# Kernel tuning notes

Hardware: AMD Instinct MI355X
Metric: run time of the kernel (lower is better)

The kernel has to match this reference:

```python
import jax, jax.numpy as jnp
import numpy as np


def _lstm_layer(x_seq, h0, c0, Wih, Whh, bih, bhh):
    """Standard (PyTorch-gate-order: i, f, g, o) LSTM over a [T, B, C] sequence."""
    b = bih + bhh  # [4H]
    # Precompute input projections for all timesteps at once: [T, B, 4H]
    x_proj = jnp.einsum('tbc,gc->tbg', x_seq, Wih) + b

    def step(carry, xp_t):
        h, c = carry
        gates = xp_t + h @ Whh.T  # [B, 4H]
        i, f, g, o = jnp.split(gates, 4, axis=-1)
        i = jax.nn.sigmoid(i)
        f = jax.nn.sigmoid(f)
        g = jnp.tanh(g)
        o = jax.nn.sigmoid(o)
        c_new = f * c + i * g
        h_new = o * jnp.tanh(c_new)
        return (h_new, c_new), h_new

    (hT, cT), ys = jax.lax.scan(step, (h0, c0), x_proj)
    return ys, hT, cT


def setup_inputs() -> dict:
    key = jax.random.key(0)
    ks = jax.random.split(key, 16)
    T, B, C, H = 1024, 64, 256, 512
    s_in = 1.0 / np.sqrt(H)
    inp = {
        'x': jax.random.normal(ks[0], (T, B, C), jnp.float32),
        'h0_0': jax.random.normal(ks[1], (B, H), jnp.float32) * 0.1,
        'c0_0': jax.random.normal(ks[2], (B, H), jnp.float32) * 0.1,
        'h0_1': jax.random.normal(ks[3], (B, H), jnp.float32) * 0.1,
        'c0_1': jax.random.normal(ks[4], (B, H), jnp.float32) * 0.1,
        'Wih0': jax.random.normal(ks[5], (4 * H, C), jnp.float32) * s_in,
        'Whh0': jax.random.normal(ks[6], (4 * H, H), jnp.float32) * s_in,
        'bih0': jax.random.normal(ks[7], (4 * H,), jnp.float32) * s_in,
        'bhh0': jax.random.normal(ks[8], (4 * H,), jnp.float32) * s_in,
        'Wih1': jax.random.normal(ks[9], (4 * H, H), jnp.float32) * s_in,
        'Whh1': jax.random.normal(ks[10], (4 * H, H), jnp.float32) * s_in,
        'bih1': jax.random.normal(ks[11], (4 * H,), jnp.float32) * s_in,
        'bhh1': jax.random.normal(ks[12], (4 * H,), jnp.float32) * s_in,
    }
    return inp


def reference(x, h0_0, c0_0, h0_1, c0_1, Wih0, Whh0, bih0, bhh0, Wih1, Whh1, bih1, bhh1):
    # Layer 0 over the full sequence, then layer 1 consumes its outputs.
    # Mathematically identical to the original timestep-major Python loop.
    y0, h1f, c1f = _lstm_layer(x, h0_0, c0_0, Wih0, Whh0, bih0, bhh0)
    y1, h2f, c2f = _lstm_layer(y0, h0_1, c0_1, Wih1, Whh1, bih1, bhh1)
    return (y1, h1f, c1f, h2f, c2f)
```

## Files before the change

kernel.cpp:

```cpp
#include <hip/hip_runtime.h>


#define TT 1024
#define BB 64
#define CC 256
#define HH 512
#define Y_ELEMS (TT * BB * HH)
#define S_ELEMS (BB * HH)

typedef __attribute__((ext_vector_type(8))) short bf16x8;
typedef __attribute__((ext_vector_type(4))) float f32x4;
typedef unsigned int u32;
typedef unsigned short u16;
typedef unsigned long long u64;

#define WS_BAR 0
#define WS_CNT 32768
#define WS_BSUM0 36864
#define WS_BSUM1 45056
#define WS_H0 53248
#define WS_H1 184320
#define WS_WPK0 315392
#define WS_WPK1 3461120

__device__ __forceinline__ u16 f2b_rne(float f) {
    u32 u = __float_as_uint(f);
    return (u16)((u + 0x7FFFu + ((u >> 16) & 1u)) >> 16);
}
__device__ __forceinline__ u16 f2b_fast(float f) {
    return (u16)((__float_as_uint(f) + 0x8000u) >> 16);
}
__device__ __forceinline__ float sigf(float z) { return 1.0f / (1.0f + __expf(-z)); }
__device__ __forceinline__ float tanh_f(float z) { return 2.0f / (1.0f + __expf(-2.0f * z)) - 1.0f; }

__device__ __forceinline__ bf16x8 pack8(float4 a, float4 b) {
    union { u16 u[8]; bf16x8 v; } r;
    r.u[0] = f2b_fast(a.x); r.u[1] = f2b_fast(a.y); r.u[2] = f2b_fast(a.z); r.u[3] = f2b_fast(a.w);
    r.u[4] = f2b_fast(b.x); r.u[5] = f2b_fast(b.y); r.u[6] = f2b_fast(b.z); r.u[7] = f2b_fast(b.w);
    return r.v;
}

__device__ __forceinline__ u32 ld_u32_sc(const u32* p) {
    return __hip_atomic_load(p, __ATOMIC_RELAXED, __HIP_MEMORY_SCOPE_AGENT);
}
__device__ __forceinline__ void add_u32_sc(u32* p, u32 v) {
    (void)__hip_atomic_fetch_add(p, v, __ATOMIC_RELAXED, __HIP_MEMORY_SCOPE_AGENT);
}

__global__ void k_init(const float* __restrict__ bih0, const float* __restrict__ bhh0,
                       const float* __restrict__ bih1, const float* __restrict__ bhh1,
                       const float* __restrict__ h00, const float* __restrict__ h01,
                       unsigned char* __restrict__ ws) {
    u32* bar = (u32*)(ws + WS_BAR);
    float* bs0 = (float*)(ws + WS_BSUM0);
    float* bs1 = (float*)(ws + WS_BSUM1);
    u16* h0 = (u16*)(ws + WS_H0);
    u16* h1 = (u16*)(ws + WS_H1);
    int t = blockIdx.x * 256 + threadIdx.x;
    if (t < 8704) bar[t] = 0u;
    if (t < 2048) { bs0[t] = bih0[t] + bhh0[t]; bs1[t] = bih1[t] + bhh1[t]; }
    if (t < S_ELEMS) {
        int b = t >> 9, col = t & 511;
        int no = ((col >> 4) << 10) + (b << 4) + (col & 15);
        h0[no] = f2b_rne(h00[t]);
        h1[no] = f2b_rne(h01[t]);
    }
}

__global__ void k_wprep(const float* __restrict__ Wih0, const float* __restrict__ Whh0,
                        const float* __restrict__ Wih1, const float* __restrict__ Whh1,
                        unsigned char* __restrict__ ws) {
    u16* wpk0 = (u16*)(ws + WS_WPK0);
    u16* wpk1 = (u16*)(ws + WS_WPK1);
    int u = blockIdx.x * 256 + threadIdx.x;
    const float* s;
    u16* d;
    if (u < 128 * 24 * 64) {
        int bidL = u / (24 * 64);
        int kt = (u >> 6) % 24;
        int lane = u & 63;
        int n = lane & 15, quad = lane >> 4;
        int row = (n >> 2) * 512 + bidL * 4 + (n & 3);
        int k = kt * 32 + quad * 8;
        s = (k < 256) ? (Wih0 + (size_t)row * 256 + k) : (Whh0 + (size_t)row * 512 + (k - 256));
        d = wpk0 + (size_t)((bidL * 24 + kt) * 64 + lane) * 8;
    } else {
        int v = u - 128 * 24 * 64;
        int bidL = v / (32 * 64);
        int kt = (v >> 6) % 32;
        int lane = v & 63;
        int n = lane & 15, quad = lane >> 4;
        int row = (n >> 2) * 512 + bidL * 4 + (n & 3);
        int k = kt * 32 + quad * 8;
        s = (k < 512) ? (Wih1 + (size_t)row * 512 + k) : (Whh1 + (size_t)row * 512 + (k - 512));
        d = wpk1 + (size_t)((bidL * 32 + kt) * 64 + lane) * 8;
    }
    #pragma unroll
    for (int i = 0; i < 8; ++i) d[i] = f2b_rne(s[i]);
}

template <int LAYER>
__device__ void run_ticks(const float* __restrict__ x, const float* __restrict__ c0,
                          float* __restrict__ out, unsigned char* __restrict__ ws,
                          int bidL, unsigned char* lds) {
    constexpr int NKT = (LAYER == 0) ? 24 : 32;
    constexpr int NL = (LAYER == 0) ? 4 : 8;
    u32* cnt = (u32*)(ws + WS_CNT);
    const float* bs = (const float*)(ws + (LAYER == 0 ? WS_BSUM0 : WS_BSUM1));
    u16* h0base = (u16*)(ws + WS_H0);
    u16* h1base = (u16*)(ws + WS_H1);
    const u16* wpk = (const u16*)(ws + (LAYER == 0 ? WS_WPK0 : WS_WPK1));

    const int bg = bidL >> 5;
    const int cg = bidL & 31;
    const int tid = threadIdx.x, lane = tid & 63, wave = tid >> 6;
    const int r16 = lane & 15, quad = lane >> 4, q8 = quad * 8;
    const int gg = r16 >> 2, jj = r16 & 3;
    const int col = cg * 16 + wave * 4 + jj;
    const int mb = quad * 4 + gg;
    const int myb = bg * 16 + mb;
    const int sl0 = (quad << 4) | (0 << 2) | jj;
    const int sl1 = (quad << 4) | (1 << 2) | jj;
    const int sl2 = (quad << 4) | (2 << 2) | jj;
    const int sl3 = (quad << 4) | (3 << 2) | jj;
    const int baseln = (quad << 4) | (gg << 2);

    u16* hstage = (u16*)(lds + 32768);
    const int sw = (r16 & 7) << 4;

    u32* gcnt = cnt + (u32)bg * 4 * 32;
    u32* mycnt = gcnt + (u32)((LAYER * 32 + cg) & 3) * 32;

    const float bi = bs[0 * HH + col], bf_ = bs[1 * HH + col];
    const float bg_ = bs[2 * HH + col], bo = bs[3 * HH + col];
    float c = c0[myb * HH + col];

    f32x4 wf[NKT];
    {
        const u16* wp = wpk + (size_t)((cg * 4 + wave) * NKT * 64 + lane) * 8;
        #pragma unroll
        for (int kt = 0; kt < NKT; ++kt) wf[kt] = *(const f32x4*)(wp + (size_t)kt * 64 * 8);
        #pragma unroll
        for (int kt = 0; kt < NKT; ++kt) asm volatile("" : "+v"(wf[kt]));
    }

    float4 xf0[8], xf1[8];
    if (LAYER == 0) {
        const float* xp = x + (size_t)(bg * 16 + r16) * CC + q8;
        #pragma unroll
        for (int kt = 0; kt < 8; ++kt) {
            xf0[kt] = *(const float4*)(xp + kt * 32);
            xf1[kt] = *(const float4*)(xp + kt * 32 + 4);
        }
    }

    for (int i = 0; i <= TT; ++i) {
        const bool active = (LAYER == 0) ? (i < TT) : (i >= 1);
        const int t = (LAYER == 0) ? i : i - 1;
        float h = 0.f;
        if (active) {
            f32x4 stg[NL];
            {
                const char* srcA = (const char*)(h0base + (size_t)((LAYER == 0 ? t : t + 1) & 1) * S_ELEMS);
                const char* srcB = (const char*)(h1base + (size_t)(t & 1) * S_ELEMS);
                #pragma unroll
                for (int k = 0; k < NL; ++k) {
                    int g = (k & 3) * 4096 + tid * 16;
                    int cgi = g >> 9;
                    int off = g & 511;
                    const char* sp = ((LAYER == 1 && k >= 4) ? srcB : srcA)
                                   + (size_t)cgi * 2048 + bg * 512 + off;
                    asm volatile("global_load_dwordx4 %0, %1, off sc0 sc1"
                                 : "=&v"(stg[k]) : "v"(sp) : "memory");
                }
            }
            f32x4 a0 = {0.f,0.f,0.f,0.f}, a1 = {0.f,0.f,0.f,0.f};
            f32x4 a2 = {0.f,0.f,0.f,0.f}, a3 = {0.f,0.f,0.f,0.f};
            if (LAYER == 0) {
                #pragma unroll
                for (int kt = 0; kt < 8; ++kt) {
                    bf16x8 a = pack8(xf0[kt], xf1[kt]);
                    bf16x8 wv = __builtin_bit_cast(bf16x8, wf[kt]);
                    f32x4& dst = (kt & 2) ? ((kt & 1) ? a3 : a2) : ((kt & 1) ? a1 : a0);
                    dst = __builtin_amdgcn_mfma_f32_16x16x32_bf16(a, wv, dst, 0, 0, 0);
                }
            }
            asm volatile("s_waitcnt vmcnt(0)" ::: "memory");
            #pragma unroll
            for (int k = 0; k < NL; ++k) {
                int g = (k & 3) * 4096 + tid * 16;
                int cgi = g >> 9;
                int off = g & 511;
                int m = off >> 5;
                int lo = (cgi * 32 + (off & 16)) ^ ((m & 7) << 4);
                int base = (LAYER == 1 && k >= 4) ? 16384 : 0;
                *(f32x4*)(lds + base + m * 1024 + lo) = stg[k];
            }
            __syncthreads();
            if (LAYER == 0) {
                #pragma unroll
                for (int kc = 0; kc < 16; kc += 8) {
                    bf16x8 av[8];
                    #pragma unroll
                    for (int j = 0; j < 8; ++j) {
                        int kt = kc + j;
                        int lo2 = (kt * 64 + quad * 16) ^ sw;
                        av[j] = *(const bf16x8*)(lds + r16 * 1024 + lo2);
                    }
                    #pragma unroll
                    for (int j = 0; j < 8; ++j) {
                        int kt = kc + j;
                        bf16x8 wv = __builtin_bit_cast(bf16x8, wf[8 + kt]);
                        f32x4& dst = (kt & 2) ? ((kt & 1) ? a3 : a2) : ((kt & 1) ? a1 : a0);
                        dst = __builtin_amdgcn_mfma_f32_16x16x32_bf16(av[j], wv, dst, 0, 0, 0);
                    }
                }
            } else {
                #pragma unroll
                for (int kc = 0; kc < 32; kc += 8) {
                    bf16x8 av[8];
                    #pragma unroll
                    for (int j = 0; j < 8; ++j) {
                        int kt = kc + j;
                        int base = (kt < 16) ? 0 : 16384;
                        int lo2 = ((kt & 15) * 64 + quad * 16) ^ sw;
                        av[j] = *(const bf16x8*)(lds + base + r16 * 1024 + lo2);
                    }
                    #pragma unroll
                    for (int j = 0; j < 8; ++j) {
                        int kt = kc + j;
                        bf16x8 wv = __builtin_bit_cast(bf16x8, wf[kt]);
                        f32x4& dst = (kt & 2) ? ((kt & 1) ? a3 : a2) : ((kt & 1) ? a1 : a0);
                        dst = __builtin_amdgcn_mfma_f32_16x16x32_bf16(av[j], wv, dst, 0, 0, 0);
                    }
                }
            }
            f32x4 acc = (a0 + a1) + (a2 + a3);

            float gi = 0.f, gf = 0.f, gc = 0.f, go = 0.f;
            #pragma unroll
            for (int r = 0; r < 4; ++r) {
                float v0 = __shfl(acc[r], sl0, 64);
                float v1 = __shfl(acc[r], sl1, 64);
                float v2 = __shfl(acc[r], sl2, 64);
                float v3 = __shfl(acc[r], sl3, 64);
                if (r == gg) { gi = v0; gf = v1; gc = v2; go = v3; }
            }
            gi = sigf(gi + bi);
            gf = sigf(gf + bf_);
            gc = tanh_f(gc + bg_);
            go = sigf(go + bo);
            c = gf * c + gi * gc;
            h = go * tanh_f(c);

            u32 w0 = f2b_rne(h);
            u32 w1 = (u32)__shfl((int)w0, baseln + 1, 64);
            u32 w2 = (u32)__shfl((int)w0, baseln + 2, 64);
            u32 w3 = (u32)__shfl((int)w0, baseln + 3, 64);
            if (jj == 0) {
                u64 pkd = (u64)(w0 | (w1 << 16)) | ((u64)(w2 | (w3 << 16)) << 32);
                *(u64*)((char*)hstage + mb * 32 + wave * 8) = pkd;
            }
        }
        if (i < TT) {
            __syncthreads();
            if (active && tid < 32) {
                u16* hw = (LAYER == 0 ? h0base : h1base) + (size_t)((t + 1) & 1) * S_ELEMS;
                f32x4 v = *(const f32x4*)((const char*)hstage + tid * 16);
                const char* dp = (const char*)hw + (size_t)cg * 2048 + bg * 512 + tid * 16;
                asm volatile("global_store_dwordx4 %0, %1, off sc0 sc1"
                             :: "v"(dp), "v"(v) : "memory");
            }
            asm volatile("s_waitcnt vmcnt(0)" ::: "memory");
            __syncthreads();
            if (tid == 0) add_u32_sc(mycnt, 1u);
        }
        if (active) {
            if (LAYER == 1) {
                float o1 = __shfl(h, baseln + 1, 64);
                float o2 = __shfl(h, baseln + 2, 64);
                float o3 = __shfl(h, baseln + 3, 64);
                if (jj == 0) {
                    float4 ov = { h, o1, o2, o3 };
                    *(float4*)(out + (size_t)t * S_ELEMS + (size_t)myb * HH
                               + cg * 16 + wave * 4) = ov;
                }
            }
            if (t == TT - 1) {
                float* fin = out + Y_ELEMS + (LAYER == 0 ? 0 : 2) * S_ELEMS;
                fin[myb * HH + col] = h;
                fin[S_ELEMS + myb * HH + col] = c;
            }
        }
        if (LAYER == 0 && i + 1 < TT) {
            const float* xp = x + ((size_t)(i + 1) * BB + bg * 16 + r16) * CC + q8;
            #pragma unroll
            for (int kt = 0; kt < 8; ++kt) {
                xf0[kt] = *(const float4*)(xp + kt * 32);
                xf1[kt] = *(const float4*)(xp + kt * 32 + 4);
            }
        }
        if (i < TT) {
            const u32 tgt = (u32)(i + 1) * 16u;
            if (tid == 0) {
                while (true) {
                    u32 v0 = ld_u32_sc(gcnt + 0 * 32);
                    u32 v1 = ld_u32_sc(gcnt + 1 * 32);
                    u32 v2 = ld_u32_sc(gcnt + 2 * 32);
                    u32 v3 = ld_u32_sc(gcnt + 3 * 32);
                    u32 m = min(min(v0, v1), min(v2, v3));
                    if (m >= tgt) break;
                }
            }
            __syncthreads();
        }
    }
}

__global__ __launch_bounds__(256) __attribute__((amdgpu_waves_per_eu(1, 1)))
void k_lstm(const float* __restrict__ x,
            const float* __restrict__ c00,
            const float* __restrict__ c01,
            float* __restrict__ out,
            unsigned char* __restrict__ ws) {
    __shared__ __align__(16) unsigned char lds[33280];
    const int bid = blockIdx.x;
    if (bid < 128) run_ticks<0>(x, c00, out, ws, bid, lds);
    else           run_ticks<1>(x, c01, out, ws, bid - 128, lds);
}

extern "C" void kernel_launch(void* const* d_in, const int* in_sizes, int n_in,
                              void* d_out, int out_size, void* d_ws, size_t ws_size,
                              hipStream_t stream) {
    const float* x    = (const float*)d_in[0];
    const float* h0_0 = (const float*)d_in[1];
    const float* c0_0 = (const float*)d_in[2];
    const float* h0_1 = (const float*)d_in[3];
    const float* c0_1 = (const float*)d_in[4];
    const float* Wih0 = (const float*)d_in[5];
    const float* Whh0 = (const float*)d_in[6];
    const float* bih0 = (const float*)d_in[7];
    const float* bhh0 = (const float*)d_in[8];
    const float* Wih1 = (const float*)d_in[9];
    const float* Whh1 = (const float*)d_in[10];
    const float* bih1 = (const float*)d_in[11];
    const float* bhh1 = (const float*)d_in[12];
    float* out = (float*)d_out;
    unsigned char* ws = (unsigned char*)d_ws;

    k_init<<<128, 256, 0, stream>>>(bih0, bhh0, bih1, bhh1, h0_0, h0_1, ws);
    k_wprep<<<1792, 256, 0, stream>>>(Wih0, Whh0, Wih1, Whh1, ws);
    k_lstm<<<256, 256, 0, stream>>>(x, c0_0, c0_1, out, ws);
}
```

Measured before the change: 4.573 ms.

## Decouple LSTM layers with slack ring buffer and direct h stores

```diff
diff --git a/kernel.cpp b/kernel.cpp
--- a/kernel.cpp
+++ b/kernel.cpp
@@ -7,6 +7,7 @@
 #define HH 512
 #define Y_ELEMS (TT * BB * HH)
 #define S_ELEMS (BB * HH)
+#define H_SLOT 65536
 
 typedef __attribute__((ext_vector_type(8))) short bf16x8;
 typedef __attribute__((ext_vector_type(4))) float f32x4;
@@ -14,14 +15,6 @@
 typedef unsigned short u16;
 typedef unsigned long long u64;
 
-#define WS_BAR 0
-#define WS_CNT 32768
-#define WS_BSUM0 36864
-#define WS_BSUM1 45056
-#define WS_H0 53248
-#define WS_H1 184320
-#define WS_WPK0 315392
-#define WS_WPK1 3461120
 
 __device__ __forceinline__ u16 f2b_rne(float f) {
     u32 u = __float_as_uint(f);
@@ -50,18 +43,17 @@
 __global__ void k_init(const float* __restrict__ bih0, const float* __restrict__ bhh0,
                        const float* __restrict__ bih1, const float* __restrict__ bhh1,
                        const float* __restrict__ h00, const float* __restrict__ h01,
-                       unsigned char* __restrict__ ws) {
-    u32* bar = (u32*)(ws + WS_BAR);
-    float* bs0 = (float*)(ws + WS_BSUM0);
-    float* bs1 = (float*)(ws + WS_BSUM1);
-    u16* h0 = (u16*)(ws + WS_H0);
-    u16* h1 = (u16*)(ws + WS_H1);
+                       unsigned char* __restrict__ ws, u64 h1off) {
+    float* bs0 = (float*)(ws + 4096);
+    float* bs1 = (float*)(ws + 12288);
+    u16* h0 = (u16*)(ws + 20480);
+    u16* h1 = (u16*)(ws + h1off);
     int t = blockIdx.x * 256 + threadIdx.x;
-    if (t < 8704) bar[t] = 0u;
+    if (t < 1024) ((u32*)ws)[t] = 0u;
     if (t < 2048) { bs0[t] = bih0[t] + bhh0[t]; bs1[t] = bih1[t] + bhh1[t]; }
     if (t < S_ELEMS) {
         int b = t >> 9, col = t & 511;
-        int no = ((col >> 4) << 10) + (b << 4) + (col & 15);
+        int no = ((col >> 4) << 10) + (((col >> 2) & 3) << 8) + (b << 2) + (col & 3);
         h0[no] = f2b_rne(h00[t]);
         h1[no] = f2b_rne(h01[t]);
     }
@@ -69,9 +61,9 @@
 
 __global__ void k_wprep(const float* __restrict__ Wih0, const float* __restrict__ Whh0,
                         const float* __restrict__ Wih1, const float* __restrict__ Whh1,
-                        unsigned char* __restrict__ ws) {
-    u16* wpk0 = (u16*)(ws + WS_WPK0);
-    u16* wpk1 = (u16*)(ws + WS_WPK1);
+                        unsigned char* __restrict__ ws, u64 wpk0off, u64 wpk1off) {
+    u16* wpk0 = (u16*)(ws + wpk0off);
+    u16* wpk1 = (u16*)(ws + wpk1off);
     int u = blockIdx.x * 256 + threadIdx.x;
     const float* s;
     u16* d;
@@ -102,17 +94,16 @@
 template <int LAYER>
 __device__ void run_ticks(const float* __restrict__ x, const float* __restrict__ c0,
                           float* __restrict__ out, unsigned char* __restrict__ ws,
-                          int bidL, unsigned char* lds) {
+                          int bidL, unsigned char* lds,
+                          u32 m0, u32 slack, u64 h1off, u64 wpkoff) {
     constexpr int NKT = (LAYER == 0) ? 24 : 32;
-    constexpr int NL = (LAYER == 0) ? 4 : 8;
-    u32* cnt = (u32*)(ws + WS_CNT);
-    const float* bs = (const float*)(ws + (LAYER == 0 ? WS_BSUM0 : WS_BSUM1));
-    u16* h0base = (u16*)(ws + WS_H0);
-    u16* h1base = (u16*)(ws + WS_H1);
-    const u16* wpk = (const u16*)(ws + (LAYER == 0 ? WS_WPK0 : WS_WPK1));
-
-    const int bg = bidL >> 5;
-    const int cg = bidL & 31;
+    u32* cnt = (u32*)ws;
+    const float* bs = (const float*)(ws + (LAYER == 0 ? 4096 : 12288));
+    unsigned char* h0base = ws + 20480;
+    unsigned char* h1base = ws + h1off;
+    const u16* wpk = (const u16*)(ws + wpkoff);
+
+    const int bg = bidL >> 5, cg = bidL & 31;
     const int tid = threadIdx.x, lane = tid & 63, wave = tid >> 6;
     const int r16 = lane & 15, quad = lane >> 4, q8 = quad * 8;
     const int gg = r16 >> 2, jj = r16 & 3;
@@ -124,12 +115,10 @@
     const int sl2 = (quad << 4) | (2 << 2) | jj;
     const int sl3 = (quad << 4) | (3 << 2) | jj;
     const int baseln = (quad << 4) | (gg << 2);
-
-    u16* hstage = (u16*)(lds + 32768);
     const int sw = (r16 & 7) << 4;
 
-    u32* gcnt = cnt + (u32)bg * 4 * 32;
-    u32* mycnt = gcnt + (u32)((LAYER * 32 + cg) & 3) * 32;
+    u32* gl = cnt + (u32)bg * 4 * 32;
+    u32* mycnt = gl + (u32)(LAYER * 2 + (cg & 1)) * 32;
 
     const float bi = bs[0 * HH + col], bf_ = bs[1 * HH + col];
     const float bg_ = bs[2 * HH + col], bo = bs[3 * HH + col];
@@ -144,6 +133,18 @@
         for (int kt = 0; kt < NKT; ++kt) asm volatile("" : "+v"(wf[kt]));
     }
 
+    auto wr2 = [&](f32x4 v, int g, int base) {
+        union { f32x4 v4; u64 q[2]; } uu; uu.v4 = v;
+        int cgi = g >> 9, w = (g >> 7) & 3, rem = g & 127;
+        int a = rem >> 4;
+        #pragma unroll
+        for (int e = 0; e < 2; ++e) {
+            int m = a * 2 + e;
+            int lo = (cgi * 32 + w * 8) ^ ((m & 7) << 4);
+            *(u64*)(lds + base + m * 1024 + lo) = uu.q[e];
+        }
+    };
+
     float4 xf0[8], xf1[8];
     if (LAYER == 0) {
         const float* xp = x + (size_t)(bg * 16 + r16) * CC + q8;
@@ -159,24 +160,19 @@
         const int t = (LAYER == 0) ? i : i - 1;
         float h = 0.f;
         if (active) {
-            f32x4 stg[NL];
-            {
-                const char* srcA = (const char*)(h0base + (size_t)((LAYER == 0 ? t : t + 1) & 1) * S_ELEMS);
-                const char* srcB = (const char*)(h1base + (size_t)(t & 1) * S_ELEMS);
-                #pragma unroll
-                for (int k = 0; k < NL; ++k) {
-                    int g = (k & 3) * 4096 + tid * 16;
-                    int cgi = g >> 9;
-                    int off = g & 511;
-                    const char* sp = ((LAYER == 1 && k >= 4) ? srcB : srcA)
-                                   + (size_t)cgi * 2048 + bg * 512 + off;
-                    asm volatile("global_load_dwordx4 %0, %1, off sc0 sc1"
-                                 : "=&v"(stg[k]) : "v"(sp) : "memory");
-                }
-            }
             f32x4 a0 = {0.f,0.f,0.f,0.f}, a1 = {0.f,0.f,0.f,0.f};
             f32x4 a2 = {0.f,0.f,0.f,0.f}, a3 = {0.f,0.f,0.f,0.f};
             if (LAYER == 0) {
+                f32x4 stg[4];
+                const char* srcA = (const char*)h0base + (size_t)((u32)t & m0) * H_SLOT;
+                #pragma unroll
+                for (int k = 0; k < 4; ++k) {
+                    int g = k * 4096 + tid * 16;
+                    const char* sp = srcA + (g >> 9) * 2048 + ((g >> 7) & 3) * 512
+                                   + bg * 128 + (g & 127);
+                    asm volatile("global_load_dwordx4 %0, %1, off sc0 sc1"
+                                 : "=&v"(stg[k]) : "v"(sp) : "memory");
+                }
                 #pragma unroll
                 for (int kt = 0; kt < 8; ++kt) {
                     bf16x8 a = pack8(xf0[kt], xf1[kt]);
@@ -184,55 +180,62 @@
                     f32x4& dst = (kt & 2) ? ((kt & 1) ? a3 : a2) : ((kt & 1) ? a1 : a0);
                     dst = __builtin_amdgcn_mfma_f32_16x16x32_bf16(a, wv, dst, 0, 0, 0);
                 }
-            }
-            asm volatile("s_waitcnt vmcnt(0)" ::: "memory");
-            #pragma unroll
-            for (int k = 0; k < NL; ++k) {
-                int g = (k & 3) * 4096 + tid * 16;
-                int cgi = g >> 9;
-                int off = g & 511;
-                int m = off >> 5;
-                int lo = (cgi * 32 + (off & 16)) ^ ((m & 7) << 4);
-                int base = (LAYER == 1 && k >= 4) ? 16384 : 0;
-                *(f32x4*)(lds + base + m * 1024 + lo) = stg[k];
-            }
-            __syncthreads();
-            if (LAYER == 0) {
-                #pragma unroll
-                for (int kc = 0; kc < 16; kc += 8) {
-                    bf16x8 av[8];
-                    #pragma unroll
-                    for (int j = 0; j < 8; ++j) {
-                        int kt = kc + j;
-                        int lo2 = (kt * 64 + quad * 16) ^ sw;
-                        av[j] = *(const bf16x8*)(lds + r16 * 1024 + lo2);
-                    }
-                    #pragma unroll
-                    for (int j = 0; j < 8; ++j) {
-                        int kt = kc + j;
-                        bf16x8 wv = __builtin_bit_cast(bf16x8, wf[8 + kt]);
-                        f32x4& dst = (kt & 2) ? ((kt & 1) ? a3 : a2) : ((kt & 1) ? a1 : a0);
-                        dst = __builtin_amdgcn_mfma_f32_16x16x32_bf16(av[j], wv, dst, 0, 0, 0);
-                    }
+                asm volatile("s_waitcnt vmcnt(0)" ::: "memory");
+                __builtin_amdgcn_sched_barrier(0);
+                #pragma unroll
+                for (int k = 0; k < 4; ++k) wr2(stg[k], k * 4096 + tid * 16, 0);
+                __syncthreads();
+                #pragma unroll
+                for (int kt = 0; kt < 16; ++kt) {
+                    bf16x8 av = *(const bf16x8*)(lds + r16 * 1024 + ((kt * 64 + quad * 16) ^ sw));
+                    bf16x8 wv = __builtin_bit_cast(bf16x8, wf[8 + kt]);
+                    f32x4& dst = (kt & 2) ? ((kt & 1) ? a3 : a2) : ((kt & 1) ? a1 : a0);
+                    dst = __builtin_amdgcn_mfma_f32_16x16x32_bf16(av, wv, dst, 0, 0, 0);
                 }
             } else {
-                #pragma unroll
-                for (int kc = 0; kc < 32; kc += 8) {
-                    bf16x8 av[8];
-                    #pragma unroll
-                    for (int j = 0; j < 8; ++j) {
-                        int kt = kc + j;
-                        int base = (kt < 16) ? 0 : 16384;
-                        int lo2 = ((kt & 15) * 64 + quad * 16) ^ sw;
-                        av[j] = *(const bf16x8*)(lds + base + r16 * 1024 + lo2);
-                    }
-                    #pragma unroll
-                    for (int j = 0; j < 8; ++j) {
-                        int kt = kc + j;
-                        bf16x8 wv = __builtin_bit_cast(bf16x8, wf[kt]);
-                        f32x4& dst = (kt & 2) ? ((kt & 1) ? a3 : a2) : ((kt & 1) ? a1 : a0);
-                        dst = __builtin_amdgcn_mfma_f32_16x16x32_bf16(av[j], wv, dst, 0, 0, 0);
-                    }
+                f32x4 stgB[4], stgA[4];
+                const char* srcB = (const char*)h1base + (size_t)((u32)t & 1) * H_SLOT;
+                const char* srcA = (const char*)h0base + (size_t)((u32)(t + 1) & m0) * H_SLOT;
+                #pragma unroll
+                for (int k = 0; k < 4; ++k) {
+                    int g = k * 4096 + tid * 16;
+                    const char* sp = srcB + (g >> 9) * 2048 + ((g >> 7) & 3) * 512
+                                   + bg * 128 + (g & 127);
+                    asm volatile("global_load_dwordx4 %0, %1, off sc0 sc1"
+                                 : "=&v"(stgB[k]) : "v"(sp) : "memory");
+                }
+                #pragma unroll
+                for (int k = 0; k < 4; ++k) {
+                    int g = k * 4096 + tid * 16;
+                    const char* sp = srcA + (g >> 9) * 2048 + ((g >> 7) & 3) * 512
+                                   + bg * 128 + (g & 127);
+                    asm volatile("global_load_dwordx4 %0, %1, off sc0 sc1"
+                                 : "=&v"(stgA[k]) : "v"(sp) : "memory");
+                }
+                asm volatile("s_waitcnt vmcnt(4)" ::: "memory");
+                __builtin_amdgcn_sched_barrier(0);
+                #pragma unroll
+                for (int k = 0; k < 4; ++k) wr2(stgB[k], k * 4096 + tid * 16, 16384);
+                __syncthreads();
+                #pragma unroll
+                for (int kt = 16; kt < 32; ++kt) {
+                    bf16x8 av = *(const bf16x8*)(lds + 16384 + r16 * 1024
+                                                 + (((kt & 15) * 64 + quad * 16) ^ sw));
+                    bf16x8 wv = __builtin_bit_cast(bf16x8, wf[kt]);
+                    f32x4& dst = (kt & 2) ? ((kt & 1) ? a3 : a2) : ((kt & 1) ? a1 : a0);
+                    dst = __builtin_amdgcn_mfma_f32_16x16x32_bf16(av, wv, dst, 0, 0, 0);
+                }
+                asm volatile("s_waitcnt vmcnt(0)" ::: "memory");
+                __builtin_amdgcn_sched_barrier(0);
+                #pragma unroll
+                for (int k = 0; k < 4; ++k) wr2(stgA[k], k * 4096 + tid * 16, 0);
+                __syncthreads();
+                #pragma unroll
+                for (int kt = 0; kt < 16; ++kt) {
+                    bf16x8 av = *(const bf16x8*)(lds + r16 * 1024 + ((kt * 64 + quad * 16) ^ sw));
+                    bf16x8 wv = __builtin_bit_cast(bf16x8, wf[kt]);
+                    f32x4& dst = (kt & 2) ? ((kt & 1) ? a3 : a2) : ((kt & 1) ? a1 : a0);
+                    dst = __builtin_amdgcn_mfma_f32_16x16x32_bf16(av, wv, dst, 0, 0, 0);
                 }
             }
             f32x4 acc = (a0 + a1) + (a2 + a3);
@@ -259,18 +262,14 @@
             u32 w3 = (u32)__shfl((int)w0, baseln + 3, 64);
             if (jj == 0) {
                 u64 pkd = (u64)(w0 | (w1 << 16)) | ((u64)(w2 | (w3 << 16)) << 32);
-                *(u64*)((char*)hstage + mb * 32 + wave * 8) = pkd;
+                unsigned char* hb = (LAYER == 0)
+                    ? h0base + (size_t)((u32)(t + 1) & m0) * H_SLOT
+                    : h1base + (size_t)((u32)(t + 1) & 1) * H_SLOT;
+                u64* dp = (u64*)(hb + cg * 2048 + wave * 512 + bg * 128 + mb * 8);
+                __hip_atomic_store(dp, pkd, __ATOMIC_RELAXED, __HIP_MEMORY_SCOPE_AGENT);
             }
         }
         if (i < TT) {
-            __syncthreads();
-            if (active && tid < 32) {
-                u16* hw = (LAYER == 0 ? h0base : h1base) + (size_t)((t + 1) & 1) * S_ELEMS;
-                f32x4 v = *(const f32x4*)((const char*)hstage + tid * 16);
-                const char* dp = (const char*)hw + (size_t)cg * 2048 + bg * 512 + tid * 16;
-                asm volatile("global_store_dwordx4 %0, %1, off sc0 sc1"
-                             :: "v"(dp), "v"(v) : "memory");
-            }
             asm volatile("s_waitcnt vmcnt(0)" ::: "memory");
             __syncthreads();
             if (tid == 0) add_u32_sc(mycnt, 1u);
@@ -301,15 +300,24 @@
             }
         }
         if (i < TT) {
-            const u32 tgt = (u32)(i + 1) * 16u;
             if (tid == 0) {
+                const u32 tO = 16u * (u32)(i + 1);
+                u32 tC;
+                if (LAYER == 0) {
+                    u32 j = (u32)(i + 1);
+                    tC = (j > slack) ? 16u * (j - slack) : 0u;
+                } else {
+                    tC = tO;
+                }
                 while (true) {
-                    u32 v0 = ld_u32_sc(gcnt + 0 * 32);
-                    u32 v1 = ld_u32_sc(gcnt + 1 * 32);
-                    u32 v2 = ld_u32_sc(gcnt + 2 * 32);
-                    u32 v3 = ld_u32_sc(gcnt + 3 * 32);
-                    u32 m = min(min(v0, v1), min(v2, v3));
-                    if (m >= tgt) break;
+                    u32 a = ld_u32_sc(gl + 0);
+                    u32 b = ld_u32_sc(gl + 32);
+                    u32 e = ld_u32_sc(gl + 64);
+                    u32 d = ld_u32_sc(gl + 96);
+                    u32 mA = min(a, b), mB = min(e, d);
+                    bool ok = (LAYER == 0) ? (mA >= tO && mB >= tC)
+                                           : (mA >= tO && mB >= tC);
+                    if (ok) break;
                 }
             }
             __syncthreads();
@@ -322,11 +330,12 @@
             const float* __restrict__ c00,
             const float* __restrict__ c01,
             float* __restrict__ out,
-            unsigned char* __restrict__ ws) {
-    __shared__ __align__(16) unsigned char lds[33280];
+            unsigned char* __restrict__ ws,
+            u32 m0, u32 slack, u64 h1off, u64 wpk0off, u64 wpk1off) {
+    __shared__ __align__(16) unsigned char lds[32768];
     const int bid = blockIdx.x;
-    if (bid < 128) run_ticks<0>(x, c00, out, ws, bid, lds);
-    else           run_ticks<1>(x, c01, out, ws, bid - 128, lds);
+    if (bid < 128) run_ticks<0>(x, c00, out, ws, bid, lds, m0, slack, h1off, wpk0off);
+    else           run_ticks<1>(x, c01, out, ws, bid - 128, lds, m0, slack, h1off, wpk1off);
 }
 
 extern "C" void kernel_launch(void* const* d_in, const int* in_sizes, int n_in,
@@ -348,7 +357,16 @@
     float* out = (float*)d_out;
     unsigned char* ws = (unsigned char*)d_ws;
 
-    k_init<<<128, 256, 0, stream>>>(bih0, bhh0, bih1, bhh1, h0_0, h0_1, ws);
-    k_wprep<<<1792, 256, 0, stream>>>(Wih0, Whh0, Wih1, Whh1, ws);
-    k_lstm<<<256, 256, 0, stream>>>(x, c0_0, c0_1, out, ws);
-}
+    const u64 NEED4 = 20480ull + 6ull * H_SLOT + 3145728ull + 4194304ull + 131072ull;
+    const bool big = (u64)ws_size >= NEED4;
+    const u32 m0 = big ? 3u : 1u;
+    const u32 slack = big ? 2u : 0u;
+    const u64 h0off = 20480ull;
+    const u64 h1off = h0off + (u64)(m0 + 1u) * H_SLOT;
+    const u64 wpk0off = h1off + 2ull * H_SLOT;
+    const u64 wpk1off = wpk0off + 3145728ull;
+
+    k_init<<<128, 256, 0, stream>>>(bih0, bhh0, bih1, bhh1, h0_0, h0_1, ws, h1off);
+    k_wprep<<<1792, 256, 0, stream>>>(Wih0, Whh0, Wih1, Whh1, ws, wpk0off, wpk1off);
+    k_lstm<<<256, 256, 0, stream>>>(x, c0_0, c0_1, out, ws, m0, slack, h1off, wpk0off, wpk1off);
+}
```

New measurement: 4.728 ms. 1.03x slower.
